# Optimization experiments

Hardware: AMD Instinct MI355X
Metric: run time of the kernel (lower is better)

Reference implementation:

```python
import jax, jax.numpy as jnp
import numpy as np

V, E, H, NL = 32000, 400, 1152, 3  # vocab, embed, hidden, layers
T, B = 64, 48


def _uniform(key, shape, std):
    return jax.random.uniform(key, shape, jnp.float32, -std, std)


def setup_inputs() -> dict:
    key = jax.random.key(0)
    ks = jax.random.split(key, 18)
    std = 1.0 / np.sqrt(H)
    inp = {
        "x": jax.random.randint(ks[0], (T, B), 0, V),
        "h0": jnp.zeros((NL, B, H), jnp.float32),
        "c0": jnp.zeros((NL, B, H), jnp.float32),
        "emb_W": jax.random.normal(ks[1], (V, E), jnp.float32) * 0.02,
        # layer 0: input E -> 4H ; layers 1,2: H -> 4H
        "W_i0": _uniform(ks[2], (4 * H, E), std), "b_i0": _uniform(ks[3], (4 * H,), std),
        "W_h0": _uniform(ks[4], (4 * H, H), std), "b_h0": _uniform(ks[5], (4 * H,), std),
        "W_i1": _uniform(ks[6], (4 * H, H), std), "b_i1": _uniform(ks[7], (4 * H,), std),
        "W_h1": _uniform(ks[8], (4 * H, H), std), "b_h1": _uniform(ks[9], (4 * H,), std),
        "W_i2": _uniform(ks[10], (4 * H, H), std), "b_i2": _uniform(ks[11], (4 * H,), std),
        "W_h2": _uniform(ks[12], (4 * H, H), std), "b_h2": _uniform(ks[13], (4 * H,), std),
        "W_dec": _uniform(ks[14], (V, H), 1.0 / np.sqrt(H)),
        "b_dec": _uniform(ks[15], (V,), 1.0 / np.sqrt(H)),
    }
    return inp


def _cell(z, h, c, Wi, bi, Wh, bh):
    # preact: [B, 4H]; gate layout per the original: i | f | o | g
    p = z @ Wi.T + bi + h @ Wh.T + bh
    i = jax.nn.sigmoid(p[:, :H])
    f = jax.nn.sigmoid(p[:, H:2 * H])
    o = jax.nn.sigmoid(p[:, 2 * H:3 * H])
    g = jnp.tanh(p[:, 3 * H:])
    c_t = f * c + i * g
    h_t = o * jnp.tanh(c_t)
    return h_t, c_t


def reference(x, h0, c0, emb_W,
              W_i0, b_i0, W_h0, b_h0,
              W_i1, b_i1, W_h1, b_h1,
              W_i2, b_i2, W_h2, b_h2,
              W_dec, b_dec):
    # eval-mode forward: dropout / drop-connect / variational dropout are identity
    emb = emb_W[x]  # [T, B, E]

    def step(carry, xt):
        ha, ca, hb, cb, hc, cc = carry
        ha, ca = _cell(xt, ha, ca, W_i0, b_i0, W_h0, b_h0)
        hb, cb = _cell(ha, hb, cb, W_i1, b_i1, W_h1, b_h1)
        hc, cc = _cell(hb, hc, cc, W_i2, b_i2, W_h2, b_h2)
        return (ha, ca, hb, cb, hc, cc), hc

    carry0 = (h0[0], c0[0], h0[1], c0[1], h0[2], c0[2])
    (ha, ca, hb, cb, hc, cc), out = jax.lax.scan(step, carry0, emb)  # out: [T, B, H]
    decoded = jnp.einsum('tbh,vh->tbv', out, W_dec) + b_dec  # [T, B, V]
    h_fin = jnp.stack([ha, hb, hc])
    c_fin = jnp.stack([ca, cb, cc])
    return decoded, (h_fin, c_fin)
```

## Files before the change

kernel.cpp:

```cpp
#include <hip/hip_runtime.h>

typedef unsigned short u16;
typedef __attribute__((ext_vector_type(8))) short s16x8;
typedef __attribute__((ext_vector_type(4))) float f32x4;

#define T_ 64
#define B_ 48
#define H_ 1152
#define E_ 400
#define EPAD 416
#define V_ 32000
#define FOURH 4608
#define TB_ 3072
#define HB (B_*H_)
#define LSTRIDE (65*HB)
#define RBLK 1024
#define PSZ ((size_t)(3*B_*FOURH))

#define OFF_ZPRE0 ((size_t)0)
#define OFF_HHI   ((size_t)56623104)
#define OFF_HLO   ((size_t)78188544)
#define OFF_CST   ((size_t)99753984)
#define OFF_ZH    ((size_t)100417536)
#define OFF_ZL    ((size_t)102973440)
#define OFF_P0    ((size_t)105529344)
#define OFF_CTR   ((size_t)116146176)

__device__ __forceinline__ u16 f2bf(float x) {
    unsigned u = __float_as_uint(x);
    u += 0x7fffu + ((u >> 16) & 1u);
    return (u16)(u >> 16);
}
__device__ __forceinline__ float bf2f(u16 h) {
    return __uint_as_float(((unsigned)h) << 16);
}
__device__ __forceinline__ void split8(const float* p, s16x8& hi, s16x8& lo) {
    f32x4 a = *(const f32x4*)(p);
    f32x4 b = *(const f32x4*)(p + 4);
    float v[8];
#pragma unroll
    for (int j = 0; j < 4; ++j) { v[j] = a[j]; v[j + 4] = b[j]; }
#pragma unroll
    for (int j = 0; j < 8; ++j) {
        u16 h = f2bf(v[j]);
        hi[j] = (short)h;
        lo[j] = (short)f2bf(v[j] - bf2f(h));
    }
}
__device__ __forceinline__ void split8r(f32x4 a, f32x4 b, s16x8& hi, s16x8& lo) {
    float v[8];
#pragma unroll
    for (int j = 0; j < 4; ++j) { v[j] = a[j]; v[j + 4] = b[j]; }
#pragma unroll
    for (int j = 0; j < 8; ++j) {
        u16 h = f2bf(v[j]);
        hi[j] = (short)h;
        lo[j] = (short)f2bf(v[j] - bf2f(h));
    }
}
__device__ __forceinline__ f32x4 mfma16(s16x8 a, s16x8 b, f32x4 c) {
    return __builtin_amdgcn_mfma_f32_16x16x32_bf16(a, b, c, 0, 0, 0);
}

__device__ __forceinline__ float ld_sc(const float* p) {
    return __hip_atomic_load(p, __ATOMIC_RELAXED, __HIP_MEMORY_SCOPE_AGENT);
}
__device__ __forceinline__ void st_sc(float* p, float v) {
    __hip_atomic_store(p, v, __ATOMIC_RELAXED, __HIP_MEMORY_SCOPE_AGENT);
}
__device__ __forceinline__ void st_sc16(u16* p, u16 v) {
    __hip_atomic_store(p, v, __ATOMIC_RELAXED, __HIP_MEMORY_SCOPE_AGENT);
}

__device__ __forceinline__ void grid_barrier(int* ctrs, int nblk) {
    asm volatile("s_waitcnt vmcnt(0)" ::: "memory");
    __syncthreads();
    if (threadIdx.x == 0) {
        int* gen = ctrs + 252;
        int* root = ctrs + 248;
        int* gcnt = ctrs + ((blockIdx.x & 15) << 4);
        const int gsz = nblk >> 4;
        int g = __hip_atomic_load(gen, __ATOMIC_RELAXED, __HIP_MEMORY_SCOPE_AGENT);
        int old = __hip_atomic_fetch_add(gcnt, 1, __ATOMIC_RELAXED, __HIP_MEMORY_SCOPE_AGENT);
        if (old == gsz - 1) {
            __hip_atomic_store(gcnt, 0, __ATOMIC_RELAXED, __HIP_MEMORY_SCOPE_AGENT);
            asm volatile("s_waitcnt vmcnt(0)" ::: "memory");
            int r = __hip_atomic_fetch_add(root, 1, __ATOMIC_RELAXED, __HIP_MEMORY_SCOPE_AGENT);
            if (r == 15) {
                __hip_atomic_store(root, 0, __ATOMIC_RELAXED, __HIP_MEMORY_SCOPE_AGENT);
                asm volatile("s_waitcnt vmcnt(0)" ::: "memory");
                __hip_atomic_fetch_add(gen, 1, __ATOMIC_RELAXED, __HIP_MEMORY_SCOPE_AGENT);
            }
        }
        while (__hip_atomic_load(gen, __ATOMIC_RELAXED, __HIP_MEMORY_SCOPE_AGENT) == g) {
            __builtin_amdgcn_s_sleep(4);
        }
    }
    __syncthreads();
}

__global__ void gather_split_kernel(const int* __restrict__ x, const float* __restrict__ embW,
                                    u16* __restrict__ Zh, u16* __restrict__ Zl) {
    int i = blockIdx.x * blockDim.x + threadIdx.x;
    const int total = TB_ * EPAD;
    if (i >= total) return;
    int tb = i / EPAD, k = i - tb * EPAD;
    float v = 0.f;
    if (k < E_) v = embW[(size_t)x[tb] * E_ + k];
    u16 h = f2bf(v);
    Zh[i] = h;
    Zl[i] = f2bf(v - bf2f(h));
}

__global__ void init_state_kernel(const float* __restrict__ h0, const float* __restrict__ c0,
                                  u16* __restrict__ Hhi, u16* __restrict__ Hlo,
                                  float* __restrict__ Cst) {
    int i = blockIdx.x * blockDim.x + threadIdx.x;
    if (i >= 3 * HB) return;
    int l = i / HB, r = i - l * HB;
    float h = h0[i];
    u16 hh = f2bf(h);
    size_t idx = (size_t)l * LSTRIDE + r;
    Hhi[idx] = hh;
    Hlo[idx] = f2bf(h - bf2f(hh));
    Cst[i] = c0[i];
}

__global__ __launch_bounds__(256, 2) void gemm_bias_kernel(
    const u16* __restrict__ Ahi, const u16* __restrict__ Alo, int lda,
    const float* __restrict__ W, int ldw, int kvalid, int ksteps,
    const float* __restrict__ bias1, const float* __restrict__ bias2,
    float* __restrict__ C, int ldc) {
    const int lane = threadIdx.x & 63;
    const int wv = threadIdx.x >> 6;
    const int m16 = lane & 15, q = lane >> 4;
    const int mbase = blockIdx.y * 192 + wv * 48;
    const int nbase = blockIdx.x * 128;

    f32x4 acc[8][3];
#pragma unroll
    for (int s8 = 0; s8 < 8; ++s8)
#pragma unroll
        for (int mt = 0; mt < 3; ++mt) acc[s8][mt] = (f32x4){0.f, 0.f, 0.f, 0.f};

    const u16* arow[3];
    const u16* alrow[3];
#pragma unroll
    for (int mt = 0; mt < 3; ++mt) {
        size_t m = (size_t)(mbase + mt * 16 + m16);
        arow[mt] = Ahi + m * lda + q * 8;
        alrow[mt] = Alo + m * lda + q * 8;
    }
    const float* wrow[8];
#pragma unroll
    for (int s8 = 0; s8 < 8; ++s8) {
        size_t n = (size_t)(nbase + s8 * 16 + m16);
        wrow[s8] = W + n * ldw + q * 8;
    }

    for (int ks = 0; ks < ksteps; ++ks) {
        int k = ks * 32;
        s16x8 ah[3], al[3];
#pragma unroll
        for (int mt = 0; mt < 3; ++mt) {
            ah[mt] = *(const s16x8*)(arow[mt] + k);
            al[mt] = *(const s16x8*)(alrow[mt] + k);
        }
        int kk = k + q * 8;
#pragma unroll
        for (int s8 = 0; s8 < 8; ++s8) {
            s16x8 wh, wl;
            if (kk + 8 <= kvalid) {
                split8(wrow[s8] + k, wh, wl);
            } else {
#pragma unroll
                for (int j = 0; j < 8; ++j) { wh[j] = 0; wl[j] = 0; }
            }
#pragma unroll
            for (int mt = 0; mt < 3; ++mt) {
                acc[s8][mt] = mfma16(ah[mt], wh, acc[s8][mt]);
                acc[s8][mt] = mfma16(ah[mt], wl, acc[s8][mt]);
                acc[s8][mt] = mfma16(al[mt], wh, acc[s8][mt]);
            }
        }
    }
#pragma unroll
    for (int s8 = 0; s8 < 8; ++s8) {
        int n = nbase + s8 * 16 + m16;
        float bv = (bias1 ? bias1[n] : 0.f) + (bias2 ? bias2[n] : 0.f);
#pragma unroll
        for (int mt = 0; mt < 3; ++mt)
#pragma unroll
            for (int r = 0; r < 4; ++r) {
                int m = mbase + mt * 16 + q * 4 + r;
                C[(size_t)m * ldc + n] = acc[s8][mt][r] + bv;
            }
    }
}

__global__ __launch_bounds__(256, 4) void recur_kernel(
    const float* __restrict__ Wh0, const float* __restrict__ Wi1, const float* __restrict__ Wh1,
    const float* __restrict__ Wi2, const float* __restrict__ Wh2,
    const float* __restrict__ bi0, const float* __restrict__ bh0,
    const float* __restrict__ bi1, const float* __restrict__ bh1,
    const float* __restrict__ bi2, const float* __restrict__ bh2,
    const float* __restrict__ Zpre0, u16* __restrict__ Hhi, u16* __restrict__ Hlo,
    float* __restrict__ Cst, float* __restrict__ P0,
    int* __restrict__ ctrs, float* __restrict__ out_h, float* __restrict__ out_c) {
    const int lane = threadIdx.x & 63;
    const int slot = threadIdx.x >> 6;
    const int blk = blockIdx.x;
    const int m16 = lane & 15, q = lane >> 4;

    for (int s = 0; s < 66; ++s) {
        const int t0 = s, t1 = s - 1, t2 = s - 2;
        int units[5];
        int nu = 0;
        if (t0 >= 0 && t0 < 64) units[nu++] = 0;
        if (t1 >= 0 && t1 < 64) { units[nu++] = 1; units[nu++] = 2; }
        if (t2 >= 0 && t2 < 64) { units[nu++] = 3; units[nu++] = 4; }
        const int ntasks = nu * 576;
        const int jj = (slot - blk) & 3;
        const int task = jj * RBLK + blk;
        if (task < ntasks) {
            const int u = units[task / 576];
            const int rem = task % 576;
            const int kh = rem & 1;
            const int strip = rem >> 1;
            const int n0 = strip * 16;
            const int koff = kh * 576;
            int tt;
            size_t aoff;
            const float* W;
            float* Pout;
            bool initZ = false;
            switch (u) {
                case 0: tt = t0; W = Wh0; aoff = (size_t)tt * HB;
                        Pout = P0 + 2 * PSZ;                          initZ = (kh == 0); break;
                case 1: tt = t1; W = Wi1; aoff = (size_t)(tt + 1) * HB;
                        Pout = P0 + (size_t)B_ * FOURH;               break;
                case 2: tt = t1; W = Wh1; aoff = LSTRIDE + (size_t)tt * HB;
                        Pout = P0 + 2 * PSZ + (size_t)B_ * FOURH;     break;
                case 3: tt = t2; W = Wi2; aoff = LSTRIDE + (size_t)(tt + 1) * HB;
                        Pout = P0 + 2 * (size_t)B_ * FOURH;           break;
                default: tt = t2; W = Wh2; aoff = 2 * (size_t)LSTRIDE + (size_t)tt * HB;
                        Pout = P0 + 2 * PSZ + 2 * (size_t)B_ * FOURH; break;
            }
            if (kh) Pout += PSZ;
            f32x4 acc[3];
            if (initZ) {
                const float* zp = Zpre0 + (size_t)(tt * B_) * FOURH + n0 + m16;
#pragma unroll
                for (int mt = 0; mt < 3; ++mt)
#pragma unroll
                    for (int r = 0; r < 4; ++r)
                        acc[mt][r] = zp[(size_t)(mt * 16 + q * 4 + r) * FOURH];
            } else {
#pragma unroll
                for (int mt = 0; mt < 3; ++mt) acc[mt] = (f32x4){0.f, 0.f, 0.f, 0.f};
            }
            const float* wrow = W + (size_t)(n0 + m16) * H_ + koff + q * 8;
            const u16* arow[3];
            const u16* alrow[3];
#pragma unroll
            for (int mt = 0; mt < 3; ++mt) {
                size_t ro = aoff + (size_t)(mt * 16 + m16) * H_ + koff + q * 8;
                arow[mt] = Hhi + ro;
                alrow[mt] = Hlo + ro;
            }
            f32x4 w0A = *(const f32x4*)(wrow);
            f32x4 w0B = *(const f32x4*)(wrow + 4);
            f32x4 w1A = *(const f32x4*)(wrow + 32);
            f32x4 w1B = *(const f32x4*)(wrow + 36);
            s16x8 ah[3], al[3];
#pragma unroll
            for (int mt = 0; mt < 3; ++mt) {
                ah[mt] = *(const s16x8*)(arow[mt]);
                al[mt] = *(const s16x8*)(alrow[mt]);
            }
#pragma unroll 2
            for (int ks = 0; ks < 18; ++ks) {
                int kp1 = ks + 1; if (kp1 > 17) kp1 = 17;
                int kp2 = ks + 2; if (kp2 > 17) kp2 = 17;
                const int kn1 = kp1 * 32, kn2 = kp2 * 32;
                f32x4 w2A = *(const f32x4*)(wrow + kn2);
                f32x4 w2B = *(const f32x4*)(wrow + kn2 + 4);
                s16x8 nah[3], nal[3];
#pragma unroll
                for (int mt = 0; mt < 3; ++mt) {
                    nah[mt] = *(const s16x8*)(arow[mt] + kn1);
                    nal[mt] = *(const s16x8*)(alrow[mt] + kn1);
                }
                s16x8 wh, wl;
                split8r(w0A, w0B, wh, wl);
#pragma unroll
                for (int mt = 0; mt < 3; ++mt) {
                    acc[mt] = mfma16(ah[mt], wh, acc[mt]);
                    acc[mt] = mfma16(ah[mt], wl, acc[mt]);
                    acc[mt] = mfma16(al[mt], wh, acc[mt]);
                }
                w0A = w1A; w0B = w1B; w1A = w2A; w1B = w2B;
#pragma unroll
                for (int mt = 0; mt < 3; ++mt) { ah[mt] = nah[mt]; al[mt] = nal[mt]; }
            }
            float* pout = Pout + n0 + m16;
#pragma unroll
            for (int mt = 0; mt < 3; ++mt)
#pragma unroll
                for (int r = 0; r < 4; ++r)
                    st_sc(pout + (size_t)(mt * 16 + q * 4 + r) * FOURH, acc[mt][r]);
        }
        grid_barrier(ctrs, RBLK);

        int actl[3];
        int nl = 0;
        if (t0 >= 0 && t0 < 64) actl[nl++] = 0;
        if (t1 >= 0 && t1 < 64) actl[nl++] = 1;
        if (t2 >= 0 && t2 < 64) actl[nl++] = 2;
        const int nitems = nl * HB;
        for (int i = blk * 256 + threadIdx.x; i < nitems; i += RBLK * 256) {
            int li = i / HB, r = i - li * HB;
            int l = actl[li];
            int tt = s - l;
            int b = r / H_, j = r - b * H_;
            const float* p2 = P0 + 2 * PSZ + (size_t)l * B_ * FOURH + (size_t)b * FOURH;
            const float* p3 = p2 + PSZ;
            float pi = ld_sc(p2 + j) + ld_sc(p3 + j);
            float pf = ld_sc(p2 + H_ + j) + ld_sc(p3 + H_ + j);
            float po = ld_sc(p2 + 2 * H_ + j) + ld_sc(p3 + 2 * H_ + j);
            float pg = ld_sc(p2 + 3 * H_ + j) + ld_sc(p3 + 3 * H_ + j);
            if (l > 0) {
                const float* pz0 = P0 + (size_t)l * B_ * FOURH + (size_t)b * FOURH;
                const float* pz1 = pz0 + PSZ;
                pi += ld_sc(pz0 + j) + ld_sc(pz1 + j);
                pf += ld_sc(pz0 + H_ + j) + ld_sc(pz1 + H_ + j);
                po += ld_sc(pz0 + 2 * H_ + j) + ld_sc(pz1 + 2 * H_ + j);
                pg += ld_sc(pz0 + 3 * H_ + j) + ld_sc(pz1 + 3 * H_ + j);
            }
            const float* bi = (l == 0) ? bi0 : (l == 1) ? bi1 : bi2;
            const float* bh = (l == 0) ? bh0 : (l == 1) ? bh1 : bh2;
            pi += bi[j] + bh[j];
            pf += bi[H_ + j] + bh[H_ + j];
            po += bi[2 * H_ + j] + bh[2 * H_ + j];
            pg += bi[3 * H_ + j] + bh[3 * H_ + j];
            float c = ld_sc(Cst + l * HB + r);
            float ig = 1.f / (1.f + expf(-pi));
            float fg = 1.f / (1.f + expf(-pf));
            float og = 1.f / (1.f + expf(-po));
            float gg = tanhf(pg);
            float cn = fg * c + ig * gg;
            float hn = og * tanhf(cn);
            st_sc(Cst + l * HB + r, cn);
            u16 hh = f2bf(hn);
            size_t hidx = (size_t)l * LSTRIDE + (size_t)(tt + 1) * HB + r;
            st_sc16(Hhi + hidx, hh);
            st_sc16(Hlo + hidx, f2bf(hn - bf2f(hh)));
            if (tt == 63) {
                out_h[l * HB + r] = hn;
                out_c[l * HB + r] = cn;
            }
        }
        grid_barrier(ctrs, RBLK);
    }
}

extern "C" void kernel_launch(void* const* d_in, const int* in_sizes, int n_in,
                              void* d_out, int out_size, void* d_ws, size_t ws_size,
                              hipStream_t stream) {
    (void)in_sizes; (void)n_in; (void)out_size; (void)ws_size;
    const int* x = (const int*)d_in[0];
    const float* h0 = (const float*)d_in[1];
    const float* c0 = (const float*)d_in[2];
    const float* embW = (const float*)d_in[3];
    const float* Wi0 = (const float*)d_in[4];
    const float* bi0 = (const float*)d_in[5];
    const float* Wh0 = (const float*)d_in[6];
    const float* bh0 = (const float*)d_in[7];
    const float* Wi1 = (const float*)d_in[8];
    const float* bi1 = (const float*)d_in[9];
    const float* Wh1 = (const float*)d_in[10];
    const float* bh1 = (const float*)d_in[11];
    const float* Wi2 = (const float*)d_in[12];
    const float* bi2 = (const float*)d_in[13];
    const float* Wh2 = (const float*)d_in[14];
    const float* bh2 = (const float*)d_in[15];
    const float* Wdec = (const float*)d_in[16];
    const float* bdec = (const float*)d_in[17];

    char* ws = (char*)d_ws;
    float* Zpre0 = (float*)(ws + OFF_ZPRE0);
    u16* Hhi = (u16*)(ws + OFF_HHI);
    u16* Hlo = (u16*)(ws + OFF_HLO);
    float* Cst = (float*)(ws + OFF_CST);
    u16* Zh = (u16*)(ws + OFF_ZH);
    u16* Zl = (u16*)(ws + OFF_ZL);
    float* P0 = (float*)(ws + OFF_P0);
    int* ctrs = (int*)(ws + OFF_CTR);

    float* decoded = (float*)d_out;
    float* out_h = decoded + (size_t)TB_ * V_;
    float* out_c = out_h + 3 * (size_t)HB;

    hipMemsetAsync(ctrs, 0, 256 * sizeof(int), stream);
    gather_split_kernel<<<(TB_ * EPAD + 255) / 256, 256, 0, stream>>>(x, embW, Zh, Zl);
    init_state_kernel<<<(3 * HB + 255) / 256, 256, 0, stream>>>(h0, c0, Hhi, Hlo, Cst);

    dim3 gA(FOURH / 128, TB_ / 192);
    gemm_bias_kernel<<<gA, 256, 0, stream>>>(Zh, Zl, EPAD, Wi0, E_, E_, (E_ + 31) / 32,
                                             nullptr, nullptr, Zpre0, FOURH);

    recur_kernel<<<RBLK, 256, 0, stream>>>(Wh0, Wi1, Wh1, Wi2, Wh2,
                                           bi0, bh0, bi1, bh1, bi2, bh2,
                                           Zpre0, Hhi, Hlo, Cst, P0, ctrs, out_h, out_c);

    dim3 gD(V_ / 128, TB_ / 192);
    gemm_bias_kernel<<<gD, 256, 0, stream>>>(Hhi + (size_t)(2 * 65 + 1) * HB,
                                             Hlo + (size_t)(2 * 65 + 1) * HB, H_,
                                             Wdec, H_, H_, H_ / 32,
                                             bdec, nullptr, decoded, V_);
}
```

Measured before the change: 7.695 ms.

## Split wavefront recurrence into per-layer persistent kernels with batched input GEMMs

```diff
diff --git a/kernel.cpp b/kernel.cpp
--- a/kernel.cpp
+++ b/kernel.cpp
@@ -14,10 +14,9 @@
 #define TB_ 3072
 #define HB (B_*H_)
 #define LSTRIDE (65*HB)
-#define RBLK 1024
-#define PSZ ((size_t)(3*B_*FOURH))
-
-#define OFF_ZPRE0 ((size_t)0)
+#define RBLK 256
+
+#define OFF_ZPRE  ((size_t)0)
 #define OFF_HHI   ((size_t)56623104)
 #define OFF_HLO   ((size_t)78188544)
 #define OFF_CST   ((size_t)99753984)
@@ -93,7 +92,7 @@
             }
         }
         while (__hip_atomic_load(gen, __ATOMIC_RELAXED, __HIP_MEMORY_SCOPE_AGENT) == g) {
-            __builtin_amdgcn_s_sleep(4);
+            __builtin_amdgcn_s_sleep(2);
         }
     }
     __syncthreads();
@@ -198,73 +197,55 @@
     }
 }
 
-__global__ __launch_bounds__(256, 4) void recur_kernel(
-    const float* __restrict__ Wh0, const float* __restrict__ Wi1, const float* __restrict__ Wh1,
-    const float* __restrict__ Wi2, const float* __restrict__ Wh2,
-    const float* __restrict__ bi0, const float* __restrict__ bh0,
-    const float* __restrict__ bi1, const float* __restrict__ bh1,
-    const float* __restrict__ bi2, const float* __restrict__ bh2,
-    const float* __restrict__ Zpre0, u16* __restrict__ Hhi, u16* __restrict__ Hlo,
-    float* __restrict__ Cst, float* __restrict__ P0,
-    int* __restrict__ ctrs, float* __restrict__ out_h, float* __restrict__ out_c) {
+__global__ __launch_bounds__(256, 2) void recur_layer_kernel(
+    const float* __restrict__ W,
+    const float* __restrict__ bi, const float* __restrict__ bh,
+    const float* __restrict__ Zpre,
+    u16* __restrict__ Hhi, u16* __restrict__ Hlo,
+    float* __restrict__ Cst,
+    float* __restrict__ P0, float* __restrict__ P1,
+    int* __restrict__ ctrs,
+    float* __restrict__ outh, float* __restrict__ outc) {
     const int lane = threadIdx.x & 63;
     const int slot = threadIdx.x >> 6;
     const int blk = blockIdx.x;
     const int m16 = lane & 15, q = lane >> 4;
-
-    for (int s = 0; s < 66; ++s) {
-        const int t0 = s, t1 = s - 1, t2 = s - 2;
-        int units[5];
-        int nu = 0;
-        if (t0 >= 0 && t0 < 64) units[nu++] = 0;
-        if (t1 >= 0 && t1 < 64) { units[nu++] = 1; units[nu++] = 2; }
-        if (t2 >= 0 && t2 < 64) { units[nu++] = 3; units[nu++] = 4; }
-        const int ntasks = nu * 576;
-        const int jj = (slot - blk) & 3;
-        const int task = jj * RBLK + blk;
-        if (task < ntasks) {
-            const int u = units[task / 576];
-            const int rem = task % 576;
-            const int kh = rem & 1;
-            const int strip = rem >> 1;
-            const int n0 = strip * 16;
-            const int koff = kh * 576;
-            int tt;
-            size_t aoff;
-            const float* W;
-            float* Pout;
-            bool initZ = false;
-            switch (u) {
-                case 0: tt = t0; W = Wh0; aoff = (size_t)tt * HB;
-                        Pout = P0 + 2 * PSZ;                          initZ = (kh == 0); break;
-                case 1: tt = t1; W = Wi1; aoff = (size_t)(tt + 1) * HB;
-                        Pout = P0 + (size_t)B_ * FOURH;               break;
-                case 2: tt = t1; W = Wh1; aoff = LSTRIDE + (size_t)tt * HB;
-                        Pout = P0 + 2 * PSZ + (size_t)B_ * FOURH;     break;
-                case 3: tt = t2; W = Wi2; aoff = LSTRIDE + (size_t)(tt + 1) * HB;
-                        Pout = P0 + 2 * (size_t)B_ * FOURH;           break;
-                default: tt = t2; W = Wh2; aoff = 2 * (size_t)LSTRIDE + (size_t)tt * HB;
-                        Pout = P0 + 2 * PSZ + 2 * (size_t)B_ * FOURH; break;
-            }
-            if (kh) Pout += PSZ;
+    const int xg = blk & 7;
+    const int li = ((blk >> 3) << 2) + slot;
+    const bool havetask = (li < 72);
+    const int strip = (li >> 1) * 8 + xg;
+    const int kh = li & 1;
+    const int n0 = strip * 16;
+    const int koff = kh * 576;
+    const float* wrow = W + (size_t)(n0 + m16) * H_ + koff + q * 8;
+    float* Pout = kh ? P1 : P0;
+    const int gi = blk * 256 + (int)threadIdx.x;
+    const int gb = gi / H_, gj = gi - gb * H_;
+
+    for (int t = 0; t < 64; ++t) {
+        if (havetask) {
+            float zin[3][4];
+            if (kh == 0) {
+                const float* zp = Zpre + (size_t)(t * B_) * FOURH + n0 + m16;
+#pragma unroll
+                for (int mt = 0; mt < 3; ++mt)
+#pragma unroll
+                    for (int r = 0; r < 4; ++r)
+                        zin[mt][r] = ld_sc(zp + (size_t)(mt * 16 + q * 4 + r) * FOURH);
+            } else {
+#pragma unroll
+                for (int mt = 0; mt < 3; ++mt)
+#pragma unroll
+                    for (int r = 0; r < 4; ++r) zin[mt][r] = 0.f;
+            }
             f32x4 acc[3];
-            if (initZ) {
-                const float* zp = Zpre0 + (size_t)(tt * B_) * FOURH + n0 + m16;
-#pragma unroll
-                for (int mt = 0; mt < 3; ++mt)
-#pragma unroll
-                    for (int r = 0; r < 4; ++r)
-                        acc[mt][r] = zp[(size_t)(mt * 16 + q * 4 + r) * FOURH];
-            } else {
-#pragma unroll
-                for (int mt = 0; mt < 3; ++mt) acc[mt] = (f32x4){0.f, 0.f, 0.f, 0.f};
-            }
-            const float* wrow = W + (size_t)(n0 + m16) * H_ + koff + q * 8;
+#pragma unroll
+            for (int mt = 0; mt < 3; ++mt) acc[mt] = (f32x4){0.f, 0.f, 0.f, 0.f};
             const u16* arow[3];
             const u16* alrow[3];
 #pragma unroll
             for (int mt = 0; mt < 3; ++mt) {
-                size_t ro = aoff + (size_t)(mt * 16 + m16) * H_ + koff + q * 8;
+                size_t ro = (size_t)t * HB + (size_t)(mt * 16 + m16) * H_ + koff + q * 8;
                 arow[mt] = Hhi + ro;
                 alrow[mt] = Hlo + ro;
             }
@@ -308,56 +289,33 @@
             for (int mt = 0; mt < 3; ++mt)
 #pragma unroll
                 for (int r = 0; r < 4; ++r)
-                    st_sc(pout + (size_t)(mt * 16 + q * 4 + r) * FOURH, acc[mt][r]);
+                    st_sc(pout + (size_t)(mt * 16 + q * 4 + r) * FOURH,
+                          acc[mt][r] + zin[mt][r]);
         }
         grid_barrier(ctrs, RBLK);
 
-        int actl[3];
-        int nl = 0;
-        if (t0 >= 0 && t0 < 64) actl[nl++] = 0;
-        if (t1 >= 0 && t1 < 64) actl[nl++] = 1;
-        if (t2 >= 0 && t2 < 64) actl[nl++] = 2;
-        const int nitems = nl * HB;
-        for (int i = blk * 256 + threadIdx.x; i < nitems; i += RBLK * 256) {
-            int li = i / HB, r = i - li * HB;
-            int l = actl[li];
-            int tt = s - l;
-            int b = r / H_, j = r - b * H_;
-            const float* p2 = P0 + 2 * PSZ + (size_t)l * B_ * FOURH + (size_t)b * FOURH;
-            const float* p3 = p2 + PSZ;
-            float pi = ld_sc(p2 + j) + ld_sc(p3 + j);
-            float pf = ld_sc(p2 + H_ + j) + ld_sc(p3 + H_ + j);
-            float po = ld_sc(p2 + 2 * H_ + j) + ld_sc(p3 + 2 * H_ + j);
-            float pg = ld_sc(p2 + 3 * H_ + j) + ld_sc(p3 + 3 * H_ + j);
-            if (l > 0) {
-                const float* pz0 = P0 + (size_t)l * B_ * FOURH + (size_t)b * FOURH;
-                const float* pz1 = pz0 + PSZ;
-                pi += ld_sc(pz0 + j) + ld_sc(pz1 + j);
-                pf += ld_sc(pz0 + H_ + j) + ld_sc(pz1 + H_ + j);
-                po += ld_sc(pz0 + 2 * H_ + j) + ld_sc(pz1 + 2 * H_ + j);
-                pg += ld_sc(pz0 + 3 * H_ + j) + ld_sc(pz1 + 3 * H_ + j);
-            }
-            const float* bi = (l == 0) ? bi0 : (l == 1) ? bi1 : bi2;
-            const float* bh = (l == 0) ? bh0 : (l == 1) ? bh1 : bh2;
-            pi += bi[j] + bh[j];
-            pf += bi[H_ + j] + bh[H_ + j];
-            po += bi[2 * H_ + j] + bh[2 * H_ + j];
-            pg += bi[3 * H_ + j] + bh[3 * H_ + j];
-            float c = ld_sc(Cst + l * HB + r);
+        if (gi < HB) {
+            const float* p0 = P0 + (size_t)gb * FOURH;
+            const float* p1 = P1 + (size_t)gb * FOURH;
+            float pi = ld_sc(p0 + gj) + ld_sc(p1 + gj) + bi[gj] + bh[gj];
+            float pf = ld_sc(p0 + H_ + gj) + ld_sc(p1 + H_ + gj) + bi[H_ + gj] + bh[H_ + gj];
+            float po = ld_sc(p0 + 2 * H_ + gj) + ld_sc(p1 + 2 * H_ + gj) + bi[2 * H_ + gj] + bh[2 * H_ + gj];
+            float pg = ld_sc(p0 + 3 * H_ + gj) + ld_sc(p1 + 3 * H_ + gj) + bi[3 * H_ + gj] + bh[3 * H_ + gj];
+            float c = ld_sc(Cst + gi);
             float ig = 1.f / (1.f + expf(-pi));
             float fg = 1.f / (1.f + expf(-pf));
             float og = 1.f / (1.f + expf(-po));
             float gg = tanhf(pg);
             float cn = fg * c + ig * gg;
             float hn = og * tanhf(cn);
-            st_sc(Cst + l * HB + r, cn);
+            st_sc(Cst + gi, cn);
             u16 hh = f2bf(hn);
-            size_t hidx = (size_t)l * LSTRIDE + (size_t)(tt + 1) * HB + r;
+            size_t hidx = (size_t)(t + 1) * HB + gi;
             st_sc16(Hhi + hidx, hh);
             st_sc16(Hlo + hidx, f2bf(hn - bf2f(hh)));
-            if (tt == 63) {
-                out_h[l * HB + r] = hn;
-                out_c[l * HB + r] = cn;
+            if (t == 63) {
+                outh[gi] = hn;
+                outc[gi] = cn;
             }
         }
         grid_barrier(ctrs, RBLK);
@@ -388,13 +346,14 @@
     const float* bdec = (const float*)d_in[17];
 
     char* ws = (char*)d_ws;
-    float* Zpre0 = (float*)(ws + OFF_ZPRE0);
+    float* Zpre = (float*)(ws + OFF_ZPRE);
     u16* Hhi = (u16*)(ws + OFF_HHI);
     u16* Hlo = (u16*)(ws + OFF_HLO);
     float* Cst = (float*)(ws + OFF_CST);
     u16* Zh = (u16*)(ws + OFF_ZH);
     u16* Zl = (u16*)(ws + OFF_ZL);
     float* P0 = (float*)(ws + OFF_P0);
+    float* P1 = P0 + (size_t)B_ * FOURH;
     int* ctrs = (int*)(ws + OFF_CTR);
 
     float* decoded = (float*)d_out;
@@ -405,13 +364,26 @@
     gather_split_kernel<<<(TB_ * EPAD + 255) / 256, 256, 0, stream>>>(x, embW, Zh, Zl);
     init_state_kernel<<<(3 * HB + 255) / 256, 256, 0, stream>>>(h0, c0, Hhi, Hlo, Cst);
 
-    dim3 gA(FOURH / 128, TB_ / 192);
-    gemm_bias_kernel<<<gA, 256, 0, stream>>>(Zh, Zl, EPAD, Wi0, E_, E_, (E_ + 31) / 32,
-                                             nullptr, nullptr, Zpre0, FOURH);
-
-    recur_kernel<<<RBLK, 256, 0, stream>>>(Wh0, Wi1, Wh1, Wi2, Wh2,
-                                           bi0, bh0, bi1, bh1, bi2, bh2,
-                                           Zpre0, Hhi, Hlo, Cst, P0, ctrs, out_h, out_c);
+    dim3 gZ(FOURH / 128, TB_ / 192);
+
+    gemm_bias_kernel<<<gZ, 256, 0, stream>>>(Zh, Zl, EPAD, Wi0, E_, E_, (E_ + 31) / 32,
+                                             nullptr, nullptr, Zpre, FOURH);
+    recur_layer_kernel<<<RBLK, 256, 0, stream>>>(Wh0, bi0, bh0, Zpre, Hhi, Hlo, Cst,
+                                                 P0, P1, ctrs, out_h, out_c);
+
+    gemm_bias_kernel<<<gZ, 256, 0, stream>>>(Hhi + HB, Hlo + HB, H_, Wi1, H_, H_, H_ / 32,
+                                             nullptr, nullptr, Zpre, FOURH);
+    recur_layer_kernel<<<RBLK, 256, 0, stream>>>(Wh1, bi1, bh1, Zpre,
+                                                 Hhi + LSTRIDE, Hlo + LSTRIDE, Cst + HB,
+                                                 P0, P1, ctrs, out_h + HB, out_c + HB);
+
+    gemm_bias_kernel<<<gZ, 256, 0, stream>>>(Hhi + LSTRIDE + HB, Hlo + LSTRIDE + HB, H_,
+                                             Wi2, H_, H_, H_ / 32,
+                                             nullptr, nullptr, Zpre, FOURH);
+    recur_layer_kernel<<<RBLK, 256, 0, stream>>>(Wh2, bi2, bh2, Zpre,
+                                                 Hhi + 2 * LSTRIDE, Hlo + 2 * LSTRIDE,
+                                                 Cst + 2 * HB,
+                                                 P0, P1, ctrs, out_h + 2 * HB, out_c + 2 * HB);
 
     dim3 gD(V_ / 128, TB_ / 192);
     gemm_bias_kernel<<<gD, 256, 0, stream>>>(Hhi + (size_t)(2 * 65 + 1) * HB,
```

New measurement: 8.816 ms. 14.6% more time.
